# Kernel tuning notes

Hardware: AMD Instinct MI355X
Metric: run time of the kernel (lower is better)

Reference implementation:

```python
import jax, jax.numpy as jnp
import numpy as np

B, S, D = 2048, 200, 64
H1, H2 = 64, 16
EPS = 1e-9
NEG_INF = -2.0**32 + 1.0


def dice(x, alpha, mean, var):
    # Dice activation at inference: BN (no center/scale) with moving stats, then
    # p = sigmoid(x_norm); out = alpha*(1-p)*x + p*x
    xn = (x - mean) * jax.lax.rsqrt(var + EPS)
    p = jax.nn.sigmoid(xn)
    return alpha * (1.0 - p) * x + p * x


def setup_inputs() -> dict:
    key = jax.random.key(0)
    ks = jax.random.split(key, 12)
    query_emb = jax.random.normal(ks[0], (B, D), dtype=jnp.float32)
    key_emb = jax.random.normal(ks[1], (B, S, D), dtype=jnp.float32)
    seq_length = jax.random.randint(ks[2], (B, 1), 1, S + 1, dtype=jnp.int32)
    # attention MLP weights (no bias): 4*D -> H1 -> H2 -> 1
    W1 = jax.random.normal(ks[3], (4 * D, H1), dtype=jnp.float32) * 0.05
    W2 = jax.random.normal(ks[4], (H1, H2), dtype=jnp.float32) * 0.05
    W3 = jax.random.normal(ks[5], (H2, 1), dtype=jnp.float32) * 0.05
    # Dice params: alpha (trainable) + BN moving stats
    alpha1 = jax.random.normal(ks[6], (H1,), dtype=jnp.float32) * 0.1
    mean1 = jax.random.normal(ks[7], (H1,), dtype=jnp.float32) * 0.1
    var1 = jax.random.uniform(ks[8], (H1,), dtype=jnp.float32, minval=0.5, maxval=1.5)
    alpha2 = jax.random.normal(ks[9], (H2,), dtype=jnp.float32) * 0.1
    mean2 = jax.random.normal(ks[10], (H2,), dtype=jnp.float32) * 0.1
    var2 = jax.random.uniform(ks[11], (H2,), dtype=jnp.float32, minval=0.5, maxval=1.5)
    return {
        "query_emb": query_emb, "key_emb": key_emb, "seq_length": seq_length,
        "W1": W1, "alpha1": alpha1, "mean1": mean1, "var1": var1,
        "W2": W2, "alpha2": alpha2, "mean2": mean2, "var2": var2,
        "W3": W3,
    }


def reference(query_emb, key_emb, seq_length, W1, alpha1, mean1, var1,
              W2, alpha2, mean2, var2, W3):
    b, s, d = key_emb.shape
    q = jnp.broadcast_to(query_emb[:, None, :], (b, s, d))
    # (B, S, 4D) interaction features
    att = jnp.concatenate([q, key_emb, q - key_emb, q * key_emb], axis=-1)
    h = dice(att @ W1, alpha1, mean1, var1)           # (B, S, H1)
    h = dice(h @ W2, alpha2, mean2, var2)             # (B, S, H2)
    score = h @ W3                                    # (B, S, 1)
    mask = (jnp.arange(s)[None, :] < seq_length).astype(score.dtype)[..., None]
    score = score * mask + (1.0 - mask) * NEG_INF
    score = jax.nn.sigmoid(score)                     # weight_normalization=False
    return jnp.sum(score * key_emb, axis=1)           # (B, D)
```

## Files before the change

### kernel.cpp

```cpp
#include <hip/hip_runtime.h>

#define NB   2048
#define SEQ  200
#define DIM  64
#define NH1  64
#define NH2  16
#define EPSF 1e-9f
#define CHUNK 64

typedef float fvec4 __attribute__((ext_vector_type(4)));
typedef short svec8 __attribute__((ext_vector_type(8)));

#define KFRAG_OFF  0
#define H1FRAG_OFF 8192
#define WROW_OFF   16384
#define QALL_OFF   16640
#define OUTP_OFF   16896
#define SMEM_BYTES 17920

__device__ __forceinline__ short f2bf(float f) {
    unsigned u = __float_as_uint(f);
    u += 0x7fffu + ((u >> 16) & 1u);
    return (short)(u >> 16);
}

__global__ __launch_bounds__(256, 4)
void din_attn_kernel(const float* __restrict__ q,
                     const float* __restrict__ key,
                     const int*   __restrict__ seqlen,
                     const float* __restrict__ W1,
                     const float* __restrict__ alpha1v,
                     const float* __restrict__ mean1v,
                     const float* __restrict__ var1v,
                     const float* __restrict__ W2,
                     const float* __restrict__ alpha2v,
                     const float* __restrict__ mean2v,
                     const float* __restrict__ var2v,
                     const float* __restrict__ W3,
                     float* __restrict__ out)
{
    __shared__ __align__(16) char smem[SMEM_BYTES];
    float* wc_t  = (float*)(smem);
    char*  kfrag = smem + KFRAG_OFF;
    char*  h1f   = smem + H1FRAG_OFF;
    float* wrowf = (float*)(smem + WROW_OFF);
    float* qall  = (float*)(smem + QALL_OFF);
    float* outp  = (float*)(smem + OUTP_OFF);
    float* qpart = (float*)(smem + OUTP_OFF);

    const int b    = blockIdx.x;
    const int t    = threadIdx.x;
    const int lane = t & 63;
    const int wave = __builtin_amdgcn_readfirstlane(t >> 6);
    const int qd4  = lane >> 4;
    const int m    = lane & 15;

    const float* qrow = q + (size_t)b * DIM;
    int nseq = seqlen[b];
    nseq = nseq < SEQ ? nseq : SEQ;

    {
        const int h = lane;
        float qt = 0.f;
        #pragma unroll
        for (int i = 0; i < 16; ++i) {
            const int d = wave * 16 + i;
            const float qdv = qrow[d];
            const float w1a = W1[(d)       * NH1 + h];
            const float w1b = W1[(64 + d)  * NH1 + h];
            const float w1c = W1[(128 + d) * NH1 + h];
            const float w1dd= W1[(192 + d) * NH1 + h];
            wc_t[d * NH1 + h] = (w1b - w1c) + qdv * w1dd;
            qt = fmaf(qdv, w1a + w1c, qt);
        }
        qpart[wave * 64 + h] = qt;
    }
    __syncthreads();

    if (t < 64)
        qall[t] = (qpart[t] + qpart[64 + t]) + (qpart[128 + t] + qpart[192 + t]);

    svec8 wcf[4][2];
    #pragma unroll
    for (int c = 0; c < 4; ++c)
        #pragma unroll
        for (int kk = 0; kk < 2; ++kk) {
            svec8 f;
            #pragma unroll
            for (int j = 0; j < 8; ++j) {
                const int d = kk * 32 + qd4 * 8 + j;
                f[j] = f2bf(wc_t[d * NH1 + (c * 16 + m)]);
            }
            wcf[c][kk] = f;
        }

    svec8 w2f[2];
    #pragma unroll
    for (int kk = 0; kk < 2; ++kk) {
        svec8 f;
        #pragma unroll
        for (int j = 0; j < 8; ++j) {
            const int h = kk * 32 + qd4 * 8 + j;
            f[j] = f2bf(W2[h * NH2 + m]);
        }
        w2f[kk] = f;
    }

    float a1v[4], m1v[4], r1v[4];
    #pragma unroll
    for (int c = 0; c < 4; ++c) {
        a1v[c] = alpha1v[c * 16 + m];
        m1v[c] = mean1v[c * 16 + m];
        r1v[c] = rsqrtf(var1v[c * 16 + m] + EPSF);
    }
    const float a2s = alpha2v[m];
    const float m2s = mean2v[m];
    const float r2s = rsqrtf(var2v[m] + EPSF);
    const float w3s = W3[m];

    __syncthreads();

    float qtermv[4];
    #pragma unroll
    for (int c = 0; c < 4; ++c) qtermv[c] = qall[c * 16 + m];

    float oacc = 0.f;

    for (int base = 0; base < SEQ; base += CHUNK) {
        if (base >= nseq) break;
        const int vrows = min(CHUNK, nseq - base);

        #pragma unroll
        for (int iter = 0; iter < 4; ++iter) {
            const int F    = iter * 256 + t;
            const int m64  = F >> 4;
            const int c4   = (F & 15) * 4;
            int grow = base + m64;
            grow = grow < SEQ ? grow : SEQ - 1;
            const float* src = key + ((size_t)b * SEQ + grow) * DIM + c4;
            const float v0 = src[0], v1 = src[1], v2 = src[2], v3 = src[3];
            unsigned p0 = (unsigned short)f2bf(v0) | ((unsigned)(unsigned short)f2bf(v1) << 16);
            unsigned p1 = (unsigned short)f2bf(v2) | ((unsigned)(unsigned short)f2bf(v3) << 16);
            const int r  = m64 >> 4;
            const int kk = c4 >> 5;
            const int qq = (c4 & 31) >> 3;
            const int ln = qq * 16 + (m64 & 15);
            uint2 pk; pk.x = p0; pk.y = p1;
            *(uint2*)(kfrag + (((r << 1) + kk) << 10) + (ln << 4) + ((c4 & 7) << 1)) = pk;
        }
        __syncthreads();

        const svec8 a0 = *(const svec8*)(kfrag + (((wave << 1) + 0) << 10) + (lane << 4));
        const svec8 a1 = *(const svec8*)(kfrag + (((wave << 1) + 1) << 10) + (lane << 4));
        fvec4 acc[4];
        #pragma unroll
        for (int c = 0; c < 4; ++c) {
            acc[c] = (fvec4){0.f, 0.f, 0.f, 0.f};
            acc[c] = __builtin_amdgcn_mfma_f32_16x16x32_bf16(a0, wcf[c][0], acc[c], 0, 0, 0);
            acc[c] = __builtin_amdgcn_mfma_f32_16x16x32_bf16(a1, wcf[c][1], acc[c], 0, 0, 0);
        }

        #pragma unroll
        for (int c = 0; c < 4; ++c) {
            const int kk2 = c >> 1;
            const int qhi = (c & 1) * 2 + (m >> 3);
            #pragma unroll
            for (int reg = 0; reg < 4; ++reg) {
                const float x  = acc[c][reg] + qtermv[c];
                const float xn = (x - m1v[c]) * r1v[c];
                const float p  = 1.f / (1.f + __expf(-xn));
                const float h1 = x * (a1v[c] + p * (1.f - a1v[c]));
                const int l2 = qhi * 16 + (qd4 * 4 + reg);
                *(short*)(h1f + (((wave << 1) + kk2) << 10) + (l2 << 4) + ((m & 7) << 1))
                    = f2bf(h1);
            }
        }

        {
            const svec8 b0 = *(const svec8*)(h1f + (((wave << 1) + 0) << 10) + (lane << 4));
            const svec8 b1 = *(const svec8*)(h1f + (((wave << 1) + 1) << 10) + (lane << 4));
            fvec4 acc2 = (fvec4){0.f, 0.f, 0.f, 0.f};
            acc2 = __builtin_amdgcn_mfma_f32_16x16x32_bf16(b0, w2f[0], acc2, 0, 0, 0);
            acc2 = __builtin_amdgcn_mfma_f32_16x16x32_bf16(b1, w2f[1], acc2, 0, 0, 0);
            #pragma unroll
            for (int reg = 0; reg < 4; ++reg) {
                const float x  = acc2[reg];
                const float xn = (x - m2s) * r2s;
                const float p  = 1.f / (1.f + __expf(-xn));
                const float hd = x * (a2s + p * (1.f - a2s));
                float s = hd * w3s;
                s += __shfl_xor(s, 1);
                s += __shfl_xor(s, 2);
                s += __shfl_xor(s, 4);
                s += __shfl_xor(s, 8);
                const int sl = wave * 16 + qd4 * 4 + reg;
                if (m == 0)
                    wrowf[sl] = (sl < vrows) ? 1.f / (1.f + __expf(-s)) : 0.f;
            }
        }
        __syncthreads();

        #pragma unroll
        for (int i = 0; i < 16; ++i) {
            const int sl = wave + 4 * i;
            int grow = base + sl;
            grow = grow < SEQ ? grow : SEQ - 1;
            const float w = wrowf[sl];
            const float* krow = key + ((size_t)b * SEQ + grow) * DIM;
            oacc = fmaf(w, krow[lane], oacc);
        }
    }

    outp[wave * 64 + lane] = oacc;
    __syncthreads();
    if (t < 64) {
        out[(size_t)b * DIM + t] = (outp[t] + outp[64 + t]) +
                                   (outp[128 + t] + outp[192 + t]);
    }
}

extern "C" void kernel_launch(void* const* d_in, const int* in_sizes, int n_in,
                              void* d_out, int out_size, void* d_ws, size_t ws_size,
                              hipStream_t stream) {
    const float* q      = (const float*)d_in[0];
    const float* key    = (const float*)d_in[1];
    const int*   seqlen = (const int*)d_in[2];
    const float* W1     = (const float*)d_in[3];
    const float* alpha1 = (const float*)d_in[4];
    const float* mean1  = (const float*)d_in[5];
    const float* var1   = (const float*)d_in[6];
    const float* W2     = (const float*)d_in[7];
    const float* alpha2 = (const float*)d_in[8];
    const float* mean2  = (const float*)d_in[9];
    const float* var2   = (const float*)d_in[10];
    const float* W3     = (const float*)d_in[11];
    float* out          = (float*)d_out;

    din_attn_kernel<<<NB, 256, 0, stream>>>(q, key, seqlen, W1,
                                            alpha1, mean1, var1,
                                            W2, alpha2, mean2, var2,
                                            W3, out);
}
```

Baseline: 184.1 us.

## Give each wave independent 16-row tiles, loading keys directly into MFMA fragments

Replaces the block-wide 64-row chunk loop with per-wave 16-row tiles strided across waves. Each lane loads key rows as float4 straight into registers, converts them to bf16 A fragments, and reuses the same fp32 registers for the weighted output sum. This removes the shared-memory key staging, the block-wide barriers per chunk, and the second global read of the key rows. The cost is a cross-lane shuffle reduction at the end, and the wave-private LDS handoff for h1 and the weights relies on no explicit barrier.

Result: slower. 188.2 us (+2.2%).

```diff
diff --git a/kernel.cpp b/kernel.cpp
--- a/kernel.cpp
+++ b/kernel.cpp
@@ -6,16 +6,10 @@
 #define NH1  64
 #define NH2  16
 #define EPSF 1e-9f
-#define CHUNK 64
 
 typedef float fvec4 __attribute__((ext_vector_type(4)));
 typedef short svec8 __attribute__((ext_vector_type(8)));
 
-#define KFRAG_OFF  0
-#define H1FRAG_OFF 8192
-#define WROW_OFF   16384
-#define QALL_OFF   16640
-#define OUTP_OFF   16896
 #define SMEM_BYTES 17920
 
 __device__ __forceinline__ short f2bf(float f) {
@@ -41,12 +35,10 @@
 {
     __shared__ __align__(16) char smem[SMEM_BYTES];
     float* wc_t  = (float*)(smem);
-    char*  kfrag = smem + KFRAG_OFF;
-    char*  h1f   = smem + H1FRAG_OFF;
-    float* wrowf = (float*)(smem + WROW_OFF);
-    float* qall  = (float*)(smem + QALL_OFF);
-    float* outp  = (float*)(smem + OUTP_OFF);
-    float* qpart = (float*)(smem + OUTP_OFF);
+    float* qpart = (float*)(smem + 16384);
+    float* outp  = (float*)(smem + 16384);
+    float* qall  = (float*)(smem + 17408);
+    float* wshb  = (float*)(smem + 17664);
 
     const int b    = blockIdx.x;
     const int t    = threadIdx.x;
@@ -55,6 +47,9 @@
     const int qd4  = lane >> 4;
     const int m    = lane & 15;
 
+    short* h1w = (short*)(smem + wave * 2048);
+    float* wsw = wshb + wave * 16;
+
     const float* qrow = q + (size_t)b * DIM;
     int nseq = seqlen[b];
     nseq = nseq < SEQ ? nseq : SEQ;
@@ -65,11 +60,11 @@
         #pragma unroll
         for (int i = 0; i < 16; ++i) {
             const int d = wave * 16 + i;
-            const float qdv = qrow[d];
-            const float w1a = W1[(d)       * NH1 + h];
-            const float w1b = W1[(64 + d)  * NH1 + h];
-            const float w1c = W1[(128 + d) * NH1 + h];
-            const float w1dd= W1[(192 + d) * NH1 + h];
+            const float qdv  = qrow[d];
+            const float w1a  = W1[(d)       * NH1 + h];
+            const float w1b  = W1[(64 + d)  * NH1 + h];
+            const float w1c  = W1[(128 + d) * NH1 + h];
+            const float w1dd = W1[(192 + d) * NH1 + h];
             wc_t[d * NH1 + h] = (w1b - w1c) + qdv * w1dd;
             qt = fmaf(qdv, w1a + w1c, qt);
         }
@@ -124,95 +119,101 @@
     #pragma unroll
     for (int c = 0; c < 4; ++c) qtermv[c] = qall[c * 16 + m];
 
-    float oacc = 0.f;
-
-    for (int base = 0; base < SEQ; base += CHUNK) {
-        if (base >= nseq) break;
-        const int vrows = min(CHUNK, nseq - base);
-
-        #pragma unroll
-        for (int iter = 0; iter < 4; ++iter) {
-            const int F    = iter * 256 + t;
-            const int m64  = F >> 4;
-            const int c4   = (F & 15) * 4;
-            int grow = base + m64;
-            grow = grow < SEQ ? grow : SEQ - 1;
-            const float* src = key + ((size_t)b * SEQ + grow) * DIM + c4;
-            const float v0 = src[0], v1 = src[1], v2 = src[2], v3 = src[3];
-            unsigned p0 = (unsigned short)f2bf(v0) | ((unsigned)(unsigned short)f2bf(v1) << 16);
-            unsigned p1 = (unsigned short)f2bf(v2) | ((unsigned)(unsigned short)f2bf(v3) << 16);
-            const int r  = m64 >> 4;
-            const int kk = c4 >> 5;
-            const int qq = (c4 & 31) >> 3;
-            const int ln = qq * 16 + (m64 & 15);
-            uint2 pk; pk.x = p0; pk.y = p1;
-            *(uint2*)(kfrag + (((r << 1) + kk) << 10) + (ln << 4) + ((c4 & 7) << 1)) = pk;
-        }
-        __syncthreads();
-
-        const svec8 a0 = *(const svec8*)(kfrag + (((wave << 1) + 0) << 10) + (lane << 4));
-        const svec8 a1 = *(const svec8*)(kfrag + (((wave << 1) + 1) << 10) + (lane << 4));
+    fvec4 oacc0 = {0.f,0.f,0.f,0.f}, oacc1 = {0.f,0.f,0.f,0.f};
+    fvec4 oacc2 = {0.f,0.f,0.f,0.f}, oacc3 = {0.f,0.f,0.f,0.f};
+
+    const int ntiles = (nseq + 15) >> 4;
+    for (int tile = wave; tile < ntiles; tile += 4) {
+        const int row  = tile * 16 + m;
+        const int grow = row < SEQ ? row : SEQ - 1;
+        const float* kp = key + ((size_t)b * SEQ + grow) * DIM + qd4 * 8;
+        const fvec4 kv0 = *(const fvec4*)(kp);
+        const fvec4 kv1 = *(const fvec4*)(kp + 4);
+        const fvec4 kv2 = *(const fvec4*)(kp + 32);
+        const fvec4 kv3 = *(const fvec4*)(kp + 36);
+
+        svec8 af0, af1;
+        #pragma unroll
+        for (int j = 0; j < 4; ++j) {
+            af0[j]     = f2bf(kv0[j]);
+            af0[4 + j] = f2bf(kv1[j]);
+            af1[j]     = f2bf(kv2[j]);
+            af1[4 + j] = f2bf(kv3[j]);
+        }
+
         fvec4 acc[4];
         #pragma unroll
         for (int c = 0; c < 4; ++c) {
             acc[c] = (fvec4){0.f, 0.f, 0.f, 0.f};
-            acc[c] = __builtin_amdgcn_mfma_f32_16x16x32_bf16(a0, wcf[c][0], acc[c], 0, 0, 0);
-            acc[c] = __builtin_amdgcn_mfma_f32_16x16x32_bf16(a1, wcf[c][1], acc[c], 0, 0, 0);
+            acc[c] = __builtin_amdgcn_mfma_f32_16x16x32_bf16(af0, wcf[c][0], acc[c], 0, 0, 0);
+            acc[c] = __builtin_amdgcn_mfma_f32_16x16x32_bf16(af1, wcf[c][1], acc[c], 0, 0, 0);
         }
 
         #pragma unroll
         for (int c = 0; c < 4; ++c) {
-            const int kk2 = c >> 1;
-            const int qhi = (c & 1) * 2 + (m >> 3);
             #pragma unroll
             for (int reg = 0; reg < 4; ++reg) {
                 const float x  = acc[c][reg] + qtermv[c];
                 const float xn = (x - m1v[c]) * r1v[c];
                 const float p  = 1.f / (1.f + __expf(-xn));
                 const float h1 = x * (a1v[c] + p * (1.f - a1v[c]));
-                const int l2 = qhi * 16 + (qd4 * 4 + reg);
-                *(short*)(h1f + (((wave << 1) + kk2) << 10) + (l2 << 4) + ((m & 7) << 1))
-                    = f2bf(h1);
+                h1w[(qd4 * 4 + reg) * NH1 + c * 16 + m] = f2bf(h1);
             }
         }
 
-        {
-            const svec8 b0 = *(const svec8*)(h1f + (((wave << 1) + 0) << 10) + (lane << 4));
-            const svec8 b1 = *(const svec8*)(h1f + (((wave << 1) + 1) << 10) + (lane << 4));
-            fvec4 acc2 = (fvec4){0.f, 0.f, 0.f, 0.f};
-            acc2 = __builtin_amdgcn_mfma_f32_16x16x32_bf16(b0, w2f[0], acc2, 0, 0, 0);
-            acc2 = __builtin_amdgcn_mfma_f32_16x16x32_bf16(b1, w2f[1], acc2, 0, 0, 0);
-            #pragma unroll
-            for (int reg = 0; reg < 4; ++reg) {
-                const float x  = acc2[reg];
-                const float xn = (x - m2s) * r2s;
-                const float p  = 1.f / (1.f + __expf(-xn));
-                const float hd = x * (a2s + p * (1.f - a2s));
-                float s = hd * w3s;
-                s += __shfl_xor(s, 1);
-                s += __shfl_xor(s, 2);
-                s += __shfl_xor(s, 4);
-                s += __shfl_xor(s, 8);
-                const int sl = wave * 16 + qd4 * 4 + reg;
-                if (m == 0)
-                    wrowf[sl] = (sl < vrows) ? 1.f / (1.f + __expf(-s)) : 0.f;
+        const svec8 b0 = *(const svec8*)(h1w + m * NH1 + qd4 * 8);
+        const svec8 b1 = *(const svec8*)(h1w + m * NH1 + 32 + qd4 * 8);
+        fvec4 acc2 = (fvec4){0.f, 0.f, 0.f, 0.f};
+        acc2 = __builtin_amdgcn_mfma_f32_16x16x32_bf16(b0, w2f[0], acc2, 0, 0, 0);
+        acc2 = __builtin_amdgcn_mfma_f32_16x16x32_bf16(b1, w2f[1], acc2, 0, 0, 0);
+
+        #pragma unroll
+        for (int reg = 0; reg < 4; ++reg) {
+            const float x  = acc2[reg];
+            const float xn = (x - m2s) * r2s;
+            const float p  = 1.f / (1.f + __expf(-xn));
+            const float hd = x * (a2s + p * (1.f - a2s));
+            float s = hd * w3s;
+            s += __shfl_xor(s, 1);
+            s += __shfl_xor(s, 2);
+            s += __shfl_xor(s, 4);
+            s += __shfl_xor(s, 8);
+            if (m == 0) {
+                const int rg = tile * 16 + qd4 * 4 + reg;
+                wsw[qd4 * 4 + reg] = (rg < nseq) ? 1.f / (1.f + __expf(-s)) : 0.f;
             }
         }
-        __syncthreads();
-
-        #pragma unroll
-        for (int i = 0; i < 16; ++i) {
-            const int sl = wave + 4 * i;
-            int grow = base + sl;
-            grow = grow < SEQ ? grow : SEQ - 1;
-            const float w = wrowf[sl];
-            const float* krow = key + ((size_t)b * SEQ + grow) * DIM;
-            oacc = fmaf(w, krow[lane], oacc);
-        }
-    }
-
-    outp[wave * 64 + lane] = oacc;
+
+        const float w = wsw[m];
+        oacc0 += w * kv0;
+        oacc1 += w * kv1;
+        oacc2 += w * kv2;
+        oacc3 += w * kv3;
+    }
+
+    #pragma unroll
+    for (int e = 0; e < 4; ++e) {
+        float v0 = oacc0[e], v1 = oacc1[e], v2 = oacc2[e], v3 = oacc3[e];
+        #pragma unroll
+        for (int msk = 1; msk < 16; msk <<= 1) {
+            v0 += __shfl_xor(v0, msk);
+            v1 += __shfl_xor(v1, msk);
+            v2 += __shfl_xor(v2, msk);
+            v3 += __shfl_xor(v3, msk);
+        }
+        oacc0[e] = v0; oacc1[e] = v1; oacc2[e] = v2; oacc3[e] = v3;
+    }
+    if (m == 0) {
+        #pragma unroll
+        for (int e = 0; e < 4; ++e) {
+            outp[wave * 64 + qd4 * 8 + e]          = oacc0[e];
+            outp[wave * 64 + qd4 * 8 + 4 + e]      = oacc1[e];
+            outp[wave * 64 + 32 + qd4 * 8 + e]     = oacc2[e];
+            outp[wave * 64 + 32 + qd4 * 8 + 4 + e] = oacc3[e];
+        }
+    }
     __syncthreads();
+
     if (t < 64) {
         out[(size_t)b * DIM + t] = (outp[t] + outp[64 + t]) +
                                    (outp[128 + t] + outp[192 + t]);
```
